# Optimization experiments

Measured on AMD Instinct MI355X. Metric: run time of the kernel, lower is better.

The kernel has to match this reference:

```python
import jax, jax.numpy as jnp
import numpy as np

NEG_BIG = -1e12
ALPHA = 0.2  # LeakyReLU negative slope

def setup_inputs() -> dict:
    key = jax.random.key(0)
    k1, k2, k3, k4, k5 = jax.random.split(key, 5)
    N, F_in, F_out = 8192, 256, 128
    inp = jax.random.normal(k1, (N, F_in), dtype=jnp.float32)
    adj = jax.random.randint(k2, (N, N), 0, 2, dtype=jnp.int32)
    W = jax.random.normal(k3, (F_in, F_out), dtype=jnp.float32) * 0.05
    W_2 = jax.random.normal(k4, (F_in, F_out), dtype=jnp.float32) * 0.05
    W_3 = jax.random.normal(k5, (F_in, F_out), dtype=jnp.float32) * 0.05
    return {"inp": inp, "adj": adj, "W": W, "W_2": W_2, "W_3": W_3}

def reference(inp, adj, W, W_2, W_3):
    # h = inp @ W, h_2 = inp @ W_2  -> scores e = LeakyReLU(h @ h_2^T)  [N, N]
    h = inp @ W
    h_2 = inp @ W_2
    e = jax.nn.leaky_relu(h @ h_2.T, negative_slope=ALPHA)
    # adjacency mask, row softmax (dropout disabled: eval mode)
    attention = jax.nn.softmax(jnp.where(adj > 0, e, NEG_BIG), axis=1)
    h_3 = inp @ W_3
    h_prime = attention @ h_3
    return jax.nn.elu(h_prime)  # concat=True path
```

## Files before the change

kernel.cpp:

```cpp
#include <hip/hip_runtime.h>
#include <hip/hip_fp16.h>

#define N    8192
#define FIN  256
#define FOUT 128
#define BN   64

typedef _Float16 half8 __attribute__((ext_vector_type(8)));
typedef _Float16 half4v __attribute__((ext_vector_type(4)));
typedef float floatx4 __attribute__((ext_vector_type(4)));

__device__ __forceinline__ float exp2_fast(float x) { return __builtin_amdgcn_exp2f(x); }

__device__ __forceinline__ void gload_lds16(const void* g, void* l) {
    __builtin_amdgcn_global_load_lds(
        (const __attribute__((address_space(1))) void*)g,
        (__attribute__((address_space(3))) void*)l, 16, 0, 0);
}

__global__ __launch_bounds__(256)
void wprep_kernel(const float* __restrict__ W0,
                  const float* __restrict__ W1,
                  const float* __restrict__ W2,
                  _Float16* __restrict__ Wf)
{
    int idx  = blockIdx.x * 256 + threadIdx.x;
    int lane = idx & 63;
    int frag = idx >> 6;
    int w    = frag >> 6;
    int f    = frag & 63;
    int nt   = f >> 3, kc = f & 7;
    int quad = lane >> 4, lo16 = lane & 15;
    const float* Wp = w == 0 ? W0 : (w == 1 ? W1 : W2);
    half8 v;
#pragma unroll
    for (int jj = 0; jj < 8; jj++)
        v[jj] = (_Float16)Wp[(size_t)(kc * 32 + quad * 8 + jj) * FOUT + nt * 16 + lo16];
    *(half8*)&Wf[(size_t)idx * 8] = v;
}

__global__ __launch_bounds__(256, 2)
void gemm3_kernel(const float* __restrict__ inp,
                  const _Float16* __restrict__ Wf,
                  _Float16* __restrict__ H,
                  _Float16* __restrict__ H2,
                  _Float16* __restrict__ H3T)
{
    const int which = blockIdx.z;
    const int c0    = blockIdx.y * 64;
    const _Float16* Wfw = Wf + (size_t)which * 64 * 64 * 8;
    const int r0 = blockIdx.x * 64;
    const int tid  = threadIdx.x;
    const int wave = tid >> 6;
    const int lane = tid & 63;
    const int lo16 = lane & 15;
    const int quad = lane >> 4;
    const int r = r0 + wave * 16 + lo16;

    half8 a[8];
#pragma unroll
    for (int kc = 0; kc < 8; kc++) {
        const float* p = &inp[(size_t)r * FIN + kc * 32 + quad * 8];
        float4 v0 = *(const float4*)p;
        float4 v1 = *(const float4*)(p + 4);
        a[kc][0] = (_Float16)v0.x; a[kc][1] = (_Float16)v0.y;
        a[kc][2] = (_Float16)v0.z; a[kc][3] = (_Float16)v0.w;
        a[kc][4] = (_Float16)v1.x; a[kc][5] = (_Float16)v1.y;
        a[kc][6] = (_Float16)v1.z; a[kc][7] = (_Float16)v1.w;
    }

    floatx4 acc[4];
#pragma unroll
    for (int i = 0; i < 4; i++) acc[i] = (floatx4){0.f, 0.f, 0.f, 0.f};

#pragma unroll
    for (int kc = 0; kc < 8; kc++)
#pragma unroll
        for (int nt = 0; nt < 4; nt++) {
            int ntg = (c0 >> 4) + nt;
            half8 b = *(const half8*)&Wfw[(((size_t)ntg * 8 + kc) * 64 + lane) * 8];
            acc[nt] = __builtin_amdgcn_mfma_f32_16x16x32_f16(a[kc], b, acc[nt], 0, 0, 0);
        }

    const int arow = wave * 16 + quad * 4;
    if (which < 2) {
        _Float16* outp = which == 0 ? H : H2;
        const float scale = which == 0 ? 1.44269504f : 1.0f;
#pragma unroll
        for (int nt = 0; nt < 4; nt++)
#pragma unroll
            for (int rr = 0; rr < 4; rr++)
                outp[(size_t)(r0 + arow + rr) * FOUT + c0 + nt * 16 + lo16] =
                    (_Float16)(acc[nt][rr] * scale);
    } else {
#pragma unroll
        for (int nt = 0; nt < 4; nt++) {
            half4v v;
#pragma unroll
            for (int rr = 0; rr < 4; rr++) v[rr] = (_Float16)acc[nt][rr];
            *(half4v*)&H3T[(size_t)(c0 + nt * 16 + lo16) * N + r0 + arow] = v;
        }
    }
}

__global__ __launch_bounds__(256)
void repackKV_kernel(const _Float16* __restrict__ H2,
                     const _Float16* __restrict__ H3T,
                     _Float16* __restrict__ Kf,
                     _Float16* __restrict__ Vf)
{
    if (blockIdx.x < 512) {
        int idx  = blockIdx.x * 256 + threadIdx.x;
        int lane = idx & 63;
        int frag = idx >> 6;
        int jb = frag >> 4, f = frag & 15;
        int c = f >> 3, ntj = (f >> 2) & 1, kc = f & 3;
        int quad = lane >> 4, lo16 = lane & 15;
        int srcrow = jb * 64 + c * 32 + (lo16 >> 2) * 8 + ntj * 4 + (lo16 & 3);
        half8 v = *(const half8*)&H2[(size_t)srcrow * FOUT + kc * 32 + quad * 8];
        *(half8*)&Kf[(size_t)idx * 8] = v;
    } else {
        int idx  = (blockIdx.x - 512) * 256 + threadIdx.x;
        int lane = idx & 63;
        int frag = idx >> 6;
        int jb = frag >> 4, f = frag & 15, nt = f >> 1, kc = f & 1;
        int quad = lane >> 4, lo16 = lane & 15;
        half8 v = *(const half8*)&H3T[(size_t)(nt * 16 + lo16) * N + jb * 64 + kc * 32 + quad * 8];
        *(half8*)&Vf[(size_t)idx * 8] = v;
    }
}

template<int JS>
__global__ __launch_bounds__(512, 2)
void attn_kernel(const _Float16* __restrict__ Hq,
                 const _Float16* __restrict__ Kf,
                 const _Float16* __restrict__ Vf,
                 const int* __restrict__ adj,
                 float* __restrict__ OpartT,
                 float* __restrict__ mpart,
                 float* __restrict__ lpart)
{
    __shared__ __align__(16) _Float16 KV[2][16384];

    const int tid  = threadIdx.x;
    const int wave = tid >> 6;
    const int lane = tid & 63;
    const int lo16 = lane & 15;
    const int quad = lane >> 4;
    const int bid  = blockIdx.x;
    const int js   = bid & (JS - 1);
    const int ib   = bid / JS;
    const int iw   = ib * 128 + wave * 16;
    const int irow = iw + lo16;
    const int jbeg = js * (N / JS);
    const int NIT  = (N / JS) / BN;
    const int jb0  = jbeg >> 6;

    half8 q[4];
#pragma unroll
    for (int kc = 0; kc < 4; kc++)
        q[kc] = *(const half8*)&Hq[(size_t)irow * FOUT + kc * 32 + quad * 8];

    floatx4 O[8];
#pragma unroll
    for (int nt = 0; nt < 8; nt++) O[nt] = (floatx4){0.f, 0.f, 0.f, 0.f};
    float m_s = -1e12f, l_s = 0.f;

    const int* abase = adj + (size_t)irow * N + jbeg + quad * 8;

    int4 pv[4];
    auto LOADAV = [&](int it) {
        const int* b = abase + it * BN;
        pv[0] = *(const int4*)(b + 0);
        pv[1] = *(const int4*)(b + 4);
        pv[2] = *(const int4*)(b + 32);
        pv[3] = *(const int4*)(b + 36);
    };
    auto PACK = [&]() -> unsigned {
        unsigned m = 0;
        m |= (pv[0].x != 0) ? 1u << 0  : 0u;  m |= (pv[0].y != 0) ? 1u << 1  : 0u;
        m |= (pv[0].z != 0) ? 1u << 2  : 0u;  m |= (pv[0].w != 0) ? 1u << 3  : 0u;
        m |= (pv[1].x != 0) ? 1u << 4  : 0u;  m |= (pv[1].y != 0) ? 1u << 5  : 0u;
        m |= (pv[1].z != 0) ? 1u << 6  : 0u;  m |= (pv[1].w != 0) ? 1u << 7  : 0u;
        m |= (pv[2].x != 0) ? 1u << 8  : 0u;  m |= (pv[2].y != 0) ? 1u << 9  : 0u;
        m |= (pv[2].z != 0) ? 1u << 10 : 0u;  m |= (pv[2].w != 0) ? 1u << 11 : 0u;
        m |= (pv[3].x != 0) ? 1u << 12 : 0u;  m |= (pv[3].y != 0) ? 1u << 13 : 0u;
        m |= (pv[3].z != 0) ? 1u << 14 : 0u;  m |= (pv[3].w != 0) ? 1u << 15 : 0u;
        return m;
    };

    auto STAGE = [&](int nxt, int jbn) {
        const _Float16* gk = Kf + (size_t)jbn * 8192;
        const _Float16* gv = Vf + (size_t)jbn * 8192;
#pragma unroll
        for (int r = 0; r < 2; r++) {
            int goff = (r * 512 + tid) * 8;
            int loff = (r * 512 + wave * 64) * 8;
            gload_lds16(gk + goff, &KV[nxt][loff]);
            gload_lds16(gv + goff, &KV[nxt][8192 + loff]);
        }
    };

    STAGE(0, jb0);
    LOADAV(0);
    __syncthreads();

    auto ITER = [&](int it, int cur) {
        unsigned mcur = PACK();
        if (it + 1 < NIT) {
            STAGE(cur ^ 1, jb0 + it + 1);
            LOADAV(it + 1);
        }

        const _Float16* kb = &KV[cur][0];
        const _Float16* vb = &KV[cur][8192];

        floatx4 S[2][2];
#pragma unroll
        for (int c = 0; c < 2; c++)
#pragma unroll
            for (int ntj = 0; ntj < 2; ntj++) {
                S[c][ntj] = (floatx4){0.f, 0.f, 0.f, 0.f};
#pragma unroll
                for (int kc = 0; kc < 4; kc++) {
                    half8 kf = *(const half8*)&kb[(((c * 2 + ntj) * 4 + kc) * 64 + lane) * 8];
                    S[c][ntj] = __builtin_amdgcn_mfma_f32_16x16x32_f16(kf, q[kc], S[c][ntj], 0, 0, 0);
                }
            }

        float mx = -1e12f;
#pragma unroll
        for (int c = 0; c < 2; c++)
#pragma unroll
            for (int ntj = 0; ntj < 2; ntj++)
#pragma unroll
                for (int r = 0; r < 4; r++) {
                    float e = S[c][ntj][r];
                    e = fmaxf(e, 0.2f * e);
                    S[c][ntj][r] = e;
                    mx = fmaxf(mx, e);
                }
        mx = fmaxf(mx, __shfl_xor(mx, 16));
        mx = fmaxf(mx, __shfl_xor(mx, 32));
        if (__any(mx > m_s + 5.75f)) {
            float mn = fmaxf(m_s, mx);
            float al = exp2_fast(m_s - mn);
            m_s = mn;
            l_s *= al;
#pragma unroll
            for (int nt = 0; nt < 8; nt++)
#pragma unroll
                for (int r = 0; r < 4; r++)
                    O[nt][r] *= al;
        }

        half8 pb[2];
        float sum = 0.f;
#pragma unroll
        for (int c = 0; c < 2; c++)
#pragma unroll
            for (int ntj = 0; ntj < 2; ntj++)
#pragma unroll
                for (int r = 0; r < 4; r++) {
                    float e = S[c][ntj][r] - m_s;
                    bool bit = (mcur >> (c * 8 + ntj * 4 + r)) & 1u;
                    float p = bit ? exp2_fast(e) : 0.f;
                    sum += p;
                    pb[c][ntj * 4 + r] = (_Float16)p;
                }
        sum += __shfl_xor(sum, 16);
        sum += __shfl_xor(sum, 32);
        l_s += sum;

#pragma unroll
        for (int c = 0; c < 2; c++)
#pragma unroll
            for (int nt = 0; nt < 8; nt++) {
                half8 vf = *(const half8*)&vb[((nt * 2 + c) * 64 + lane) * 8];
                O[nt] = __builtin_amdgcn_mfma_f32_16x16x32_f16(vf, pb[c], O[nt], 0, 0, 0);
            }

        __syncthreads();
    };

    for (int it2 = 0; it2 < NIT; it2 += 2) {
        ITER(it2,     0);
        ITER(it2 + 1, 1);
    }

#pragma unroll
    for (int nt = 0; nt < 8; nt++)
#pragma unroll
        for (int r = 0; r < 4; r++) {
            int f = nt * 16 + quad * 4 + r;
            OpartT[((size_t)js * FOUT + f) * N + irow] = O[nt][r];
        }
    if (quad == 0) {
        mpart[js * N + irow] = m_s;
        lpart[js * N + irow] = l_s;
    }
}

template<int JS>
__global__ __launch_bounds__(256)
void combine_kernel(const float* __restrict__ OpartT,
                    const float* __restrict__ mpart,
                    const float* __restrict__ lpart,
                    float* __restrict__ out)
{
    int idx = blockIdx.x * 256 + threadIdx.x;
    int f  = idx >> 11;
    int i4 = (idx & 2047) << 2;

    float4 M = {-3e38f, -3e38f, -3e38f, -3e38f};
    float4 m[JS];
#pragma unroll
    for (int s = 0; s < JS; s++) {
        m[s] = *(const float4*)&mpart[s * N + i4];
        M.x = fmaxf(M.x, m[s].x); M.y = fmaxf(M.y, m[s].y);
        M.z = fmaxf(M.z, m[s].z); M.w = fmaxf(M.w, m[s].w);
    }
    float4 L = {0.f, 0.f, 0.f, 0.f};
    float4 o = {0.f, 0.f, 0.f, 0.f};
#pragma unroll
    for (int s = 0; s < JS; s++) {
        float4 l = *(const float4*)&lpart[s * N + i4];
        float4 w;
        w.x = exp2_fast(m[s].x - M.x); w.y = exp2_fast(m[s].y - M.y);
        w.z = exp2_fast(m[s].z - M.z); w.w = exp2_fast(m[s].w - M.w);
        L.x += l.x * w.x; L.y += l.y * w.y;
        L.z += l.z * w.z; L.w += l.w * w.w;
        float4 v = *(const float4*)&OpartT[((size_t)s * FOUT + f) * N + i4];
        o.x += w.x * v.x; o.y += w.y * v.y;
        o.z += w.z * v.z; o.w += w.w * v.w;
    }
    float r0 = o.x / L.x, r1 = o.y / L.y, r2 = o.z / L.z, r3 = o.w / L.w;
    out[(size_t)(i4 + 0) * FOUT + f] = r0 > 0.f ? r0 : __expf(r0) - 1.f;
    out[(size_t)(i4 + 1) * FOUT + f] = r1 > 0.f ? r1 : __expf(r1) - 1.f;
    out[(size_t)(i4 + 2) * FOUT + f] = r2 > 0.f ? r2 : __expf(r2) - 1.f;
    out[(size_t)(i4 + 3) * FOUT + f] = r3 > 0.f ? r3 : __expf(r3) - 1.f;
}

extern "C" void kernel_launch(void* const* d_in, const int* in_sizes, int n_in,
                              void* d_out, int out_size, void* d_ws, size_t ws_size,
                              hipStream_t stream) {
    const float* inp = (const float*)d_in[0];
    const int*   adj = (const int*)d_in[1];
    const float* W0  = (const float*)d_in[2];
    const float* W1  = (const float*)d_in[3];
    const float* W2  = (const float*)d_in[4];
    float* out = (float*)d_out;

    constexpr int JS = 8;
    char* ws = (char*)d_ws;
    _Float16* H    = (_Float16*)(ws);
    _Float16* H2   = (_Float16*)(ws + (2u << 20));
    _Float16* H3T  = (_Float16*)(ws + (4u << 20));
    _Float16* Wf   = (_Float16*)(ws + (6u << 20));
    _Float16* Kf   = (_Float16*)(ws + (7u << 20));
    _Float16* Vf   = (_Float16*)(ws + (9u << 20));
    float* OpartT  = (float*)(ws + (11u << 20));
    float* mpart   = (float*)(ws + (43u << 20));
    float* lpart   = (float*)(ws + (43u << 20) + (size_t)JS * N * sizeof(float));

    wprep_kernel<<<48, 256, 0, stream>>>(W0, W1, W2, Wf);
    gemm3_kernel<<<dim3(N / 64, 2, 3), 256, 0, stream>>>(inp, Wf, H, H2, H3T);
    repackKV_kernel<<<1024, 256, 0, stream>>>(H2, H3T, Kf, Vf);
    attn_kernel<JS><<<(N / 128) * JS, 512, 0, stream>>>(H, Kf, Vf, adj, OpartT, mpart, lpart);
    combine_kernel<JS><<<(FOUT * (N / 4)) / 256, 256, 0, stream>>>(OpartT, mpart, lpart, out);
}
```

Before: 423.5 us.

## Load adjacency rows coalesced and build masks via wave ballots

The adjacency tile is now read as contiguous 256-int row segments per wave, one row per load, instead of strided per-lane int4 chunks. Each wave converts these into 64-bit bitmasks with __ballot, spreads the ballot work over four iterations, and double-buffers the masks. This is meant to make the adjacency loads, the dominant memory stream, better coalesced and to cut per-lane compare and pack work. In exchange it adds more ballot instructions and 64-bit mask registers, and it hardcodes NIT=16, which ties the kernel to a specific JS value.

```diff
diff --git a/kernel.cpp b/kernel.cpp
--- a/kernel.cpp
+++ b/kernel.cpp
@@ -147,13 +147,14 @@
     const int lane = tid & 63;
     const int lo16 = lane & 15;
     const int quad = lane >> 4;
+    const int qsh  = quad * 2;
     const int bid  = blockIdx.x;
     const int js   = bid & (JS - 1);
     const int ib   = bid / JS;
     const int iw   = ib * 128 + wave * 16;
     const int irow = iw + lo16;
     const int jbeg = js * (N / JS);
-    const int NIT  = (N / JS) / BN;
+    constexpr int NIT = 16;
     const int jb0  = jbeg >> 6;
 
     half8 q[4];
@@ -166,28 +167,9 @@
     for (int nt = 0; nt < 8; nt++) O[nt] = (floatx4){0.f, 0.f, 0.f, 0.f};
     float m_s = -1e12f, l_s = 0.f;
 
-    const int* abase = adj + (size_t)irow * N + jbeg + quad * 8;
-
-    int4 pv[4];
-    auto LOADAV = [&](int it) {
-        const int* b = abase + it * BN;
-        pv[0] = *(const int4*)(b + 0);
-        pv[1] = *(const int4*)(b + 4);
-        pv[2] = *(const int4*)(b + 32);
-        pv[3] = *(const int4*)(b + 36);
-    };
-    auto PACK = [&]() -> unsigned {
-        unsigned m = 0;
-        m |= (pv[0].x != 0) ? 1u << 0  : 0u;  m |= (pv[0].y != 0) ? 1u << 1  : 0u;
-        m |= (pv[0].z != 0) ? 1u << 2  : 0u;  m |= (pv[0].w != 0) ? 1u << 3  : 0u;
-        m |= (pv[1].x != 0) ? 1u << 4  : 0u;  m |= (pv[1].y != 0) ? 1u << 5  : 0u;
-        m |= (pv[1].z != 0) ? 1u << 6  : 0u;  m |= (pv[1].w != 0) ? 1u << 7  : 0u;
-        m |= (pv[2].x != 0) ? 1u << 8  : 0u;  m |= (pv[2].y != 0) ? 1u << 9  : 0u;
-        m |= (pv[2].z != 0) ? 1u << 10 : 0u;  m |= (pv[2].w != 0) ? 1u << 11 : 0u;
-        m |= (pv[3].x != 0) ? 1u << 12 : 0u;  m |= (pv[3].y != 0) ? 1u << 13 : 0u;
-        m |= (pv[3].z != 0) ? 1u << 14 : 0u;  m |= (pv[3].w != 0) ? 1u << 15 : 0u;
-        return m;
-    };
+    const int* arow_base = adj + (size_t)iw * N + jbeg + lane * 4;
+
+    unsigned long long mA[4], mB[4];
 
     auto STAGE = [&](int nxt, int jbn) {
         const _Float16* gk = Kf + (size_t)jbn * 8192;
@@ -201,16 +183,48 @@
         }
     };
 
+    auto BALLOT4 = [&](unsigned long long (&mn)[4], int p,
+                       const int4& a0, const int4& a1, const int4& a2, const int4& a3) {
+#pragma unroll
+        for (int qq = 0; qq < 4; qq++) {
+            const int4& a = (qq == 0) ? a0 : (qq == 1) ? a1 : (qq == 2) ? a2 : a3;
+            unsigned long long b0 = __ballot(a.x != 0);
+            unsigned long long b1 = __ballot(a.y != 0);
+            unsigned long long b2 = __ballot(a.z != 0);
+            unsigned long long b3 = __ballot(a.w != 0);
+            bool sel = (lo16 == p * 4 + qq);
+            mn[0] = sel ? b0 : mn[0];
+            mn[1] = sel ? b1 : mn[1];
+            mn[2] = sel ? b2 : mn[2];
+            mn[3] = sel ? b3 : mn[3];
+        }
+    };
+
     STAGE(0, jb0);
-    LOADAV(0);
+#pragma unroll
+    for (int p = 0; p < 4; p++) {
+        const int* rb = arow_base;
+        int4 a0 = *(const int4*)(rb + (size_t)(p * 4 + 0) * N);
+        int4 a1 = *(const int4*)(rb + (size_t)(p * 4 + 1) * N);
+        int4 a2 = *(const int4*)(rb + (size_t)(p * 4 + 2) * N);
+        int4 a3 = *(const int4*)(rb + (size_t)(p * 4 + 3) * N);
+        BALLOT4(mA, p, a0, a1, a2, a3);
+    }
     __syncthreads();
 
-    auto ITER = [&](int it, int cur) {
-        unsigned mcur = PACK();
-        if (it + 1 < NIT) {
-            STAGE(cur ^ 1, jb0 + it + 1);
-            LOADAV(it + 1);
-        }
+    auto ITER = [&](int it, int p, unsigned long long (&mc)[4],
+                    unsigned long long (&mn)[4], bool buildNext, int gnext) {
+        const int cur = it & 1;
+
+        int4 a0, a1, a2, a3;
+        if (buildNext) {
+            const int* rb = arow_base + gnext * 256;
+            a0 = *(const int4*)(rb + (size_t)(p * 4 + 0) * N);
+            a1 = *(const int4*)(rb + (size_t)(p * 4 + 1) * N);
+            a2 = *(const int4*)(rb + (size_t)(p * 4 + 2) * N);
+            a3 = *(const int4*)(rb + (size_t)(p * 4 + 3) * N);
+        }
+        if (it + 1 < NIT) STAGE(cur ^ 1, jb0 + it + 1);
 
         const _Float16* kb = &KV[cur][0];
         const _Float16* vb = &KV[cur][8192];
@@ -243,9 +257,9 @@
         mx = fmaxf(mx, __shfl_xor(mx, 16));
         mx = fmaxf(mx, __shfl_xor(mx, 32));
         if (__any(mx > m_s + 5.75f)) {
-            float mn = fmaxf(m_s, mx);
-            float al = exp2_fast(m_s - mn);
-            m_s = mn;
+            float mn2 = fmaxf(m_s, mx);
+            float al = exp2_fast(m_s - mn2);
+            m_s = mn2;
             l_s *= al;
 #pragma unroll
             for (int nt = 0; nt < 8; nt++)
@@ -263,10 +277,10 @@
 #pragma unroll
                 for (int r = 0; r < 4; r++) {
                     float e = S[c][ntj][r] - m_s;
-                    bool bit = (mcur >> (c * 8 + ntj * 4 + r)) & 1u;
-                    float p = bit ? exp2_fast(e) : 0.f;
-                    sum += p;
-                    pb[c][ntj * 4 + r] = (_Float16)p;
+                    bool bit = (mc[r] >> (p * 16 + c * 8 + ntj + qsh)) & 1ull;
+                    float pp = bit ? exp2_fast(e) : 0.f;
+                    sum += pp;
+                    pb[c][ntj * 4 + r] = (_Float16)pp;
                 }
         sum += __shfl_xor(sum, 16);
         sum += __shfl_xor(sum, 32);
@@ -280,12 +294,19 @@
                 O[nt] = __builtin_amdgcn_mfma_f32_16x16x32_f16(vf, pb[c], O[nt], 0, 0, 0);
             }
 
+        if (buildNext) BALLOT4(mn, p, a0, a1, a2, a3);
+
         __syncthreads();
     };
 
-    for (int it2 = 0; it2 < NIT; it2 += 2) {
-        ITER(it2,     0);
-        ITER(it2 + 1, 1);
+#pragma unroll
+    for (int g = 0; g < 4; g++) {
+#pragma unroll
+        for (int p = 0; p < 4; p++) {
+            int it = g * 4 + p;
+            if (g & 1) ITER(it, p, mB, mA, g < 3, g + 1);
+            else       ITER(it, p, mA, mB, g < 3, g + 1);
+        }
     }
 
 #pragma unroll
```

After: 412.9 us. 2.5% less time.
